# Optimization experiments

Hardware: AMD Instinct MI355X
Metric: run time of the kernel (lower is better)

The kernel has to match this reference:

```python
import jax, jax.numpy as jnp
import numpy as np

V, D, NL, L, N = 50257, 512, 4, 2048, 32  # vocab, d_model, n_layers, seq_len, complex state modes (d_state=64)


def setup_inputs() -> dict:
    key = jax.random.key(0)
    ks = jax.random.split(key, 10)
    s = lambda k, shp, sc=1.0: jax.random.normal(k, shp, dtype=jnp.float32) * sc
    # dt log-uniform in [1e-3, 1e-1], standard S4 init; shared layout (NL, D)
    log_dt = jnp.tile(jnp.linspace(np.log(1e-3), np.log(1e-1), D, dtype=np.float32)[None], (NL, 1))
    return {
        "input_ids": jax.random.randint(ks[0], (2, L), 0, V, dtype=jnp.int64),
        "token_embed": s(ks[1], (V, D), 0.02),
        "pos_embed": s(ks[2], (L, D), 0.02),
        "log_dt": log_dt,
        "C_re": s(ks[3], (NL, D, N)),
        "C_im": s(ks[4], (NL, D, N)),
        "skip_D": s(ks[5], (NL, D)),
        "out_w": s(ks[6], (NL, 2 * D, D), 1.0 / np.sqrt(D)),
        "out_b": jnp.zeros((NL, 2 * D), jnp.float32),
        "ln_g": jnp.ones((D,), jnp.float32),
        "ln_b": jnp.zeros((D,), jnp.float32),
        "head_w": s(ks[7], (V, D), 1.0 / np.sqrt(D)),
    }


def _s4d_kernel(log_dt, C_re, C_im):
    # S4D-Lin init, ZOH discretization -> causal conv kernel (D, L)
    A = (-0.5 + 1j * jnp.pi * jnp.arange(N)).astype(jnp.complex64)      # (N,)
    dtA = jnp.exp(log_dt)[:, None] * A[None, :]                          # (D, N)
    C = (C_re + 1j * C_im).astype(jnp.complex64) * (jnp.exp(dtA) - 1.0) / A
    # Vandermonde: exp(l * dtA); (D, N, L) complex64 transient
    K = C[:, :, None] * jnp.exp(dtA[:, :, None] * jnp.arange(L))
    return 2.0 * jnp.real(K.sum(1))                                      # (D, L)


def _fft_causal_conv(u, K):
    # u: (B, L, D), K: (D, L) -> causal conv along time, per channel
    n = 2 * L
    Uf = jnp.fft.rfft(u, n=n, axis=1)            # (B, n/2+1, D)
    Kf = jnp.fft.rfft(K.T, n=n, axis=0)[None]    # (1, n/2+1, D)
    return jnp.fft.irfft(Uf * Kf, n=n, axis=1)[:, :L]


def _s4_block(x, log_dt, C_re, C_im, skip_D, out_w, out_b):
    y = _fft_causal_conv(x, _s4d_kernel(log_dt, C_re, C_im)) + x * skip_D
    y = jax.nn.gelu(y)
    z = y @ out_w.T + out_b                       # (B, L, 2D)
    return z[..., :D] * jax.nn.sigmoid(z[..., D:])  # GLU output projection


def reference(input_ids, token_embed, pos_embed, log_dt, C_re, C_im,
              skip_D, out_w, out_b, ln_g, ln_b, head_w):
    T = input_ids.shape[1]
    x = token_embed[input_ids] + pos_embed[None, :T]
    for i in range(NL):  # fixed small layer count
        x = x + _s4_block(x, log_dt[i], C_re[i], C_im[i], skip_D[i], out_w[i], out_b[i])
    mu = x.mean(-1, keepdims=True)
    var = ((x - mu) ** 2).mean(-1, keepdims=True)
    x = (x - mu) / jnp.sqrt(var + 1e-5) * ln_g + ln_b
    return x @ head_w.T  # logits (B, L, V)
```

## Files before the change

kernel.cpp:

```cpp
#include <hip/hip_runtime.h>
#include <math.h>

#define LSEQ   2048
#define DM     512
#define NLAYER 4
#define NMODE  32
#define BATCH  2
#define VOCAB  50257
#define CHUNK  32
#define NCHUNK 64
#define ROWS   (BATCH*LSEQ)
#define PI_F   3.14159265358979323846f

typedef __bf16 bf16_t;
typedef __bf16 bf16x8 __attribute__((ext_vector_type(8)));
typedef float  floatx4 __attribute__((ext_vector_type(4)));

__device__ __forceinline__ float gelu_f(float v) {
  return 0.5f * v * (1.0f + tanhf(0.7978845608028654f * (v + 0.044715f * v * v * v)));
}
__device__ __forceinline__ float sigmoid_f(float v) {
  return 1.0f / (1.0f + expf(-v));
}

__global__ __launch_bounds__(256) void prep_kernel(
    const float* __restrict__ log_dt, const float* __restrict__ C_re,
    const float* __restrict__ C_im, float* __restrict__ wcp) {
  int idx = blockIdx.x * 256 + threadIdx.x;
  int n  = idx & (NMODE - 1);
  int ld = idx >> 5;
  float dt = expf(log_dt[ld]);
  float ar = -0.5f * dt;
  float ai = PI_F * (float)n * dt;
  float em = expf(ar);
  float wr = em * cosf(ai), wi = em * sinf(ai);
  float pn = PI_F * (float)n;
  float inv = 1.0f / (0.25f + pn * pn);
  float m1r = wr - 1.0f, m1i = wi;
  float qr = (-0.5f * m1r + pn * m1i) * inv;
  float qi = (-0.5f * m1i - pn * m1r) * inv;
  float cre = C_re[idx], cim = C_im[idx];
  float cpr = cre * qr - cim * qi;
  float cpi = cre * qi + cim * qr;
  float emT = expf(ar * (float)CHUNK);
  float aT  = ai * (float)CHUNK;
  float wTr = emT * cosf(aT), wTi = emT * sinf(aT);
  float* o = wcp + (size_t)idx * 6;
  o[0] = wr; o[1] = wi; o[2] = cpr; o[3] = cpi; o[4] = wTr; o[5] = wTi;
}

__global__ __launch_bounds__(256) void embed_kernel(
    const int* __restrict__ ids, const float* __restrict__ tok,
    const float* __restrict__ pos, float* __restrict__ x) {
  int idx = blockIdx.x * 256 + threadIdx.x;
  int d  = idx & (DM - 1);
  int bl = idx >> 9;
  int l  = bl & (LSEQ - 1);
  int id = ids[bl];
  x[idx] = tok[(size_t)id * DM + d] + pos[(size_t)l * DM + d];
}

__global__ __launch_bounds__(256) void cvt_bf16_kernel(
    const float* __restrict__ src, bf16_t* __restrict__ dst, int n) {
  int idx = blockIdx.x * 256 + threadIdx.x;
  if (idx < n) dst[idx] = (bf16_t)src[idx];
}

__global__ __launch_bounds__(256) void scan_phase1_kernel(
    const float* __restrict__ x, const float* __restrict__ wcp,
    float2* __restrict__ E, int layer) {
  int idx = blockIdx.x * 256 + threadIdx.x;
  int d  = idx & (DM - 1);
  int bc = idx >> 9;
  int c  = bc & (NCHUNK - 1);
  int b  = bc >> 6;
  const float* xp = x + ((size_t)(b * LSEQ + c * CHUNK)) * DM + d;
  float xr[CHUNK];
  #pragma unroll
  for (int t = 0; t < CHUNK; t++) xr[t] = xp[(size_t)t * DM];
  const float* wp = wcp + (size_t)(layer * DM + d) * NMODE * 6;
  float2* Ep = E + ((size_t)(b * DM + d) * NCHUNK + c) * NMODE;
  #pragma unroll 1
  for (int np = 0; np < NMODE / 2; np++) {
    int n0 = np * 2;
    float w0r = wp[n0*6+0], w0i = wp[n0*6+1];
    float w1r = wp[n0*6+6], w1i = wp[n0*6+7];
    float s0r = 0.f, s0i = 0.f, s1r = 0.f, s1i = 0.f;
    #pragma unroll
    for (int t = 0; t < CHUNK; t++) {
      float xt = xr[t];
      float a0r = fmaf(w0r, s0r, fmaf(-w0i, s0i, xt));
      float a0i = fmaf(w0r, s0i, w0i * s0r);
      float a1r = fmaf(w1r, s1r, fmaf(-w1i, s1i, xt));
      float a1i = fmaf(w1r, s1i, w1i * s1r);
      s0r = a0r; s0i = a0i; s1r = a1r; s1i = a1i;
    }
    Ep[n0]     = make_float2(s0r, s0i);
    Ep[n0 + 1] = make_float2(s1r, s1i);
  }
}

__global__ __launch_bounds__(256) void scan_combine_kernel(
    const float* __restrict__ wcp, float2* __restrict__ E, int layer) {
  int idx = blockIdx.x * 256 + threadIdx.x;
  int n  = idx & (NMODE - 1);
  int bd = idx >> 5;
  int d  = bd & (DM - 1);
  const float* wp = wcp + ((size_t)(layer * DM + d) * NMODE + n) * 6;
  float wTr = wp[4], wTi = wp[5];
  float2* Ep = E + (size_t)bd * NCHUNK * NMODE + n;
  float sr = 0.f, si = 0.f;
  for (int c = 0; c < NCHUNK; c++) {
    float2 e = Ep[(size_t)c * NMODE];
    Ep[(size_t)c * NMODE] = make_float2(sr, si);
    float tr = fmaf(wTr, sr, -(wTi * si)) + e.x;
    float ti = fmaf(wTr, si, wTi * sr) + e.y;
    sr = tr; si = ti;
  }
}

__global__ __launch_bounds__(256) void scan_phase2_kernel(
    const float* __restrict__ x, const float* __restrict__ wcp,
    const float2* __restrict__ E, const float* __restrict__ skipD,
    bf16_t* __restrict__ yb, int layer) {
  int idx = blockIdx.x * 256 + threadIdx.x;
  int d  = idx & (DM - 1);
  int bc = idx >> 9;
  int c  = bc & (NCHUNK - 1);
  int b  = bc >> 6;
  const float* xp = x + ((size_t)(b * LSEQ + c * CHUNK)) * DM + d;
  float xr[CHUNK];
  #pragma unroll
  for (int t = 0; t < CHUNK; t++) xr[t] = xp[(size_t)t * DM];
  float ya[CHUNK];
  #pragma unroll
  for (int t = 0; t < CHUNK; t++) ya[t] = 0.f;
  const float* wp = wcp + (size_t)(layer * DM + d) * NMODE * 6;
  const float2* Ep = E + ((size_t)(b * DM + d) * NCHUNK + c) * NMODE;
  #pragma unroll 1
  for (int np = 0; np < NMODE / 2; np++) {
    int n0 = np * 2;
    float w0r = wp[n0*6+0], w0i = wp[n0*6+1];
    float c0r = wp[n0*6+2], c0i = wp[n0*6+3];
    float w1r = wp[n0*6+6], w1i = wp[n0*6+7];
    float c1r = wp[n0*6+8], c1i = wp[n0*6+9];
    float2 e0 = Ep[n0], e1 = Ep[n0 + 1];
    float s0r = e0.x, s0i = e0.y, s1r = e1.x, s1i = e1.y;
    #pragma unroll
    for (int t = 0; t < CHUNK; t++) {
      float xt = xr[t];
      float a0r = fmaf(w0r, s0r, fmaf(-w0i, s0i, xt));
      float a0i = fmaf(w0r, s0i, w0i * s0r);
      float a1r = fmaf(w1r, s1r, fmaf(-w1i, s1i, xt));
      float a1i = fmaf(w1r, s1i, w1i * s1r);
      s0r = a0r; s0i = a0i; s1r = a1r; s1i = a1i;
      float acc = fmaf(c0r, s0r, ya[t]);
      acc = fmaf(-c0i, s0i, acc);
      acc = fmaf(c1r, s1r, acc);
      ya[t] = fmaf(-c1i, s1i, acc);
    }
  }
  float sk = skipD[layer * DM + d];
  bf16_t* yp = yb + ((size_t)(b * LSEQ + c * CHUNK)) * DM + d;
  #pragma unroll
  for (int t = 0; t < CHUNK; t++) {
    float v = fmaf(xr[t], sk, 2.0f * ya[t]);
    yp[(size_t)t * DM] = (bf16_t)gelu_f(v);
  }
}

__global__ __launch_bounds__(256) void gemm_bt_kernel(
    const bf16_t* __restrict__ A, const bf16_t* __restrict__ B,
    float* __restrict__ C, const float* __restrict__ bias, int Nreal, int K) {
  __shared__ __align__(16) bf16_t As[128 * 32];
  __shared__ __align__(16) bf16_t Bs[128 * 32];
  int tid = threadIdx.x;
  int lid = tid & 63;
  int w   = tid >> 6;
  int tileM = blockIdx.y * 128;
  int tileN = blockIdx.x * 128;
  int wm = w & 1, wn = w >> 1;

  floatx4 acc[4][4];
  floatx4 zero = {0.f, 0.f, 0.f, 0.f};
  #pragma unroll
  for (int i = 0; i < 4; i++)
    #pragma unroll
    for (int j = 0; j < 4; j++) acc[i][j] = zero;

  for (int k0 = 0; k0 < K; k0 += 32) {
    #pragma unroll
    for (int i = 0; i < 2; i++) {
      int flat = i * 256 + tid;
      int row  = flat >> 2;
      int kg   = (flat & 3) * 8;
      const bf16_t* ga = A + (size_t)(tileM + row) * K + (k0 + kg);
      int brow = tileN + row;
      if (brow >= Nreal) brow = Nreal - 1;
      const bf16_t* gb = B + (size_t)brow * K + (k0 + kg);
      __builtin_amdgcn_global_load_lds(
          (const __attribute__((address_space(1))) void*)ga,
          (__attribute__((address_space(3))) void*)(&As[flat * 8]), 16, 0, 0);
      __builtin_amdgcn_global_load_lds(
          (const __attribute__((address_space(1))) void*)gb,
          (__attribute__((address_space(3))) void*)(&Bs[flat * 8]), 16, 0, 0);
    }
    __syncthreads();

    bf16x8 af[4], bfr[4];
    #pragma unroll
    for (int i = 0; i < 4; i++) {
      af[i]  = *(const bf16x8*)&As[((wm * 64 + i * 16 + (lid & 15)) * 32) + ((lid >> 4) * 8)];
      bfr[i] = *(const bf16x8*)&Bs[((wn * 64 + i * 16 + (lid & 15)) * 32) + ((lid >> 4) * 8)];
    }
    #pragma unroll
    for (int i = 0; i < 4; i++)
      #pragma unroll
      for (int j = 0; j < 4; j++)
        acc[i][j] = __builtin_amdgcn_mfma_f32_16x16x32_bf16(af[i], bfr[j], acc[i][j], 0, 0, 0);
    __syncthreads();
  }

  #pragma unroll
  for (int i = 0; i < 4; i++) {
    int m = tileM + wm * 64 + i * 16 + (lid >> 4) * 4;
    #pragma unroll
    for (int j = 0; j < 4; j++) {
      int n = tileN + wn * 64 + j * 16 + (lid & 15);
      if (n < Nreal) {
        float bv = bias ? bias[n] : 0.f;
        #pragma unroll
        for (int r = 0; r < 4; r++)
          C[(size_t)(m + r) * Nreal + n] = acc[i][j][r] + bv;
      }
    }
  }
}

__global__ __launch_bounds__(256) void glu_res_kernel(
    const float* __restrict__ z, float* __restrict__ x) {
  int idx = blockIdx.x * 256 + threadIdx.x;
  int d = idx & (DM - 1);
  int m = idx >> 9;
  float a = z[(size_t)m * (2 * DM) + d];
  float g = z[(size_t)m * (2 * DM) + DM + d];
  x[idx] += a * sigmoid_f(g);
}

__global__ __launch_bounds__(256) void ln_kernel(
    const float* __restrict__ x, const float* __restrict__ g,
    const float* __restrict__ bta, bf16_t* __restrict__ xn) {
  int m = blockIdx.x;
  int tid = threadIdx.x;
  int lid = tid & 63, w = tid >> 6;
  const float* xp = x + (size_t)m * DM;
  float v0 = xp[tid], v1 = xp[tid + 256];
  __shared__ float sw[4];
  __shared__ float bcast;
  float s = v0 + v1;
  #pragma unroll
  for (int o = 32; o > 0; o >>= 1) s += __shfl_down(s, o);
  if (lid == 0) sw[w] = s;
  __syncthreads();
  if (tid == 0) bcast = (sw[0] + sw[1] + sw[2] + sw[3]) * (1.0f / DM);
  __syncthreads();
  float mu = bcast;
  float d0 = v0 - mu, d1 = v1 - mu;
  float q = d0 * d0 + d1 * d1;
  #pragma unroll
  for (int o = 32; o > 0; o >>= 1) q += __shfl_down(q, o);
  __syncthreads();
  if (lid == 0) sw[w] = q;
  __syncthreads();
  if (tid == 0) bcast = rsqrtf((sw[0] + sw[1] + sw[2] + sw[3]) * (1.0f / DM) + 1e-5f);
  __syncthreads();
  float rs = bcast;
  xn[(size_t)m * DM + tid]       = (bf16_t)(d0 * rs * g[tid] + bta[tid]);
  xn[(size_t)m * DM + tid + 256] = (bf16_t)(d1 * rs * g[tid + 256] + bta[tid + 256]);
}

extern "C" void kernel_launch(void* const* d_in, const int* in_sizes, int n_in,
                              void* d_out, int out_size, void* d_ws, size_t ws_size,
                              hipStream_t stream) {
  const int*   ids   = (const int*)  d_in[0];
  const float* tok   = (const float*)d_in[1];
  const float* pos   = (const float*)d_in[2];
  const float* logdt = (const float*)d_in[3];
  const float* cre   = (const float*)d_in[4];
  const float* cim   = (const float*)d_in[5];
  const float* skipD = (const float*)d_in[6];
  const float* outw  = (const float*)d_in[7];
  const float* outb  = (const float*)d_in[8];
  const float* lng   = (const float*)d_in[9];
  const float* lnb   = (const float*)d_in[10];
  const float* headw = (const float*)d_in[11];
  float* logits = (float*)d_out;

  char* ws = (char*)d_ws;
  float*  x   = (float*)(ws);
  float*  z   = (float*)(ws + (8u  << 20));
  float2* E   = (float2*)(ws + (8u << 20));
  bf16_t* yb  = (bf16_t*)(ws + (24u << 20));
  bf16_t* xn  = (bf16_t*)(ws + (24u << 20));
  bf16_t* wb  = (bf16_t*)(ws + (28u << 20));
  float*  wcp = (float*)(ws + (32u << 20));
  bf16_t* hb  = (bf16_t*)(ws + (34u << 20));

  prep_kernel<<<(NLAYER * DM * NMODE) / 256, 256, 0, stream>>>(logdt, cre, cim, wcp);
  cvt_bf16_kernel<<<(NLAYER * 2 * DM * DM) / 256, 256, 0, stream>>>(outw, wb, NLAYER * 2 * DM * DM);
  cvt_bf16_kernel<<<(VOCAB * DM + 255) / 256, 256, 0, stream>>>(headw, hb, VOCAB * DM);
  embed_kernel<<<(ROWS * DM) / 256, 256, 0, stream>>>(ids, tok, pos, x);

  for (int layer = 0; layer < NLAYER; layer++) {
    scan_phase1_kernel<<<(BATCH * NCHUNK * DM) / 256, 256, 0, stream>>>(x, wcp, E, layer);
    scan_combine_kernel<<<(BATCH * DM * NMODE) / 256, 256, 0, stream>>>(wcp, E, layer);
    scan_phase2_kernel<<<(BATCH * NCHUNK * DM) / 256, 256, 0, stream>>>(x, wcp, E, skipD, yb, layer);
    dim3 g1((2 * DM) / 128, ROWS / 128);
    gemm_bt_kernel<<<g1, 256, 0, stream>>>(yb, wb + (size_t)layer * 2 * DM * DM, z,
                                           outb + layer * 2 * DM, 2 * DM, DM);
    glu_res_kernel<<<(ROWS * DM) / 256, 256, 0, stream>>>(z, x);
  }

  ln_kernel<<<ROWS, 256, 0, stream>>>(x, lng, lnb, xn);
  dim3 g2((VOCAB + 127) / 128, ROWS / 128);
  gemm_bt_kernel<<<g2, 256, 0, stream>>>(xn, hb, logits, nullptr, VOCAB, DM);
}
```

Before: 1.583 ms.

## Fuse GLU into output-projection GEMM, retile head GEMM, vectorize bf16 conversions

Each layer's output-projection GEMM now applies the GLU gate and residual add in its epilogue. The weight rows are permuted at conversion time so gate and value columns land in the same tile, which removes the z buffer round trip and one kernel per layer. The vocab head GEMM moves to a 256x256 tile, 512-thread kernel with 64-wide K double-buffered LDS staging, an XCD-aware block remap and MFMA priority hints. The fp32-to-bf16 conversions are vectorized to 8 elements per thread. The risks are the larger LDS footprint (128KB per block) limiting occupancy, and correctness of the row permutation.

```diff
diff --git a/kernel.cpp b/kernel.cpp
--- a/kernel.cpp
+++ b/kernel.cpp
@@ -60,10 +60,35 @@
   x[idx] = tok[(size_t)id * DM + d] + pos[(size_t)l * DM + d];
 }
 
-__global__ __launch_bounds__(256) void cvt_bf16_kernel(
-    const float* __restrict__ src, bf16_t* __restrict__ dst, int n) {
-  int idx = blockIdx.x * 256 + threadIdx.x;
-  if (idx < n) dst[idx] = (bf16_t)src[idx];
+__global__ __launch_bounds__(256) void cvt8_kernel(
+    const float* __restrict__ src, bf16_t* __restrict__ dst, int n8) {
+  int idx8 = blockIdx.x * 256 + threadIdx.x;
+  if (idx8 >= n8) return;
+  int gid = idx8 * 8;
+  float4 f0 = *(const float4*)(src + gid);
+  float4 f1 = *(const float4*)(src + gid + 4);
+  bf16x8 v;
+  v[0] = (bf16_t)f0.x; v[1] = (bf16_t)f0.y; v[2] = (bf16_t)f0.z; v[3] = (bf16_t)f0.w;
+  v[4] = (bf16_t)f1.x; v[5] = (bf16_t)f1.y; v[6] = (bf16_t)f1.z; v[7] = (bf16_t)f1.w;
+  *(bf16x8*)(dst + gid) = v;
+}
+
+__global__ __launch_bounds__(256) void cvt_wperm_kernel(
+    const float* __restrict__ src, bf16_t* __restrict__ dst) {
+  int idx8 = blockIdx.x * 256 + threadIdx.x;
+  int gid = idx8 * 8;
+  int layer = gid >> 19;
+  int rem = gid & ((1 << 19) - 1);
+  int r = rem >> 9;
+  int c = rem & 511;
+  int orig = ((r >> 4) & 1) * 512 + ((r >> 5) << 4) + (r & 15);
+  const float* s = src + ((size_t)layer << 19) + ((size_t)orig << 9) + c;
+  float4 f0 = *(const float4*)s;
+  float4 f1 = *(const float4*)(s + 4);
+  bf16x8 v;
+  v[0] = (bf16_t)f0.x; v[1] = (bf16_t)f0.y; v[2] = (bf16_t)f0.z; v[3] = (bf16_t)f0.w;
+  v[4] = (bf16_t)f1.x; v[5] = (bf16_t)f1.y; v[6] = (bf16_t)f1.z; v[7] = (bf16_t)f1.w;
+  *(bf16x8*)(dst + gid) = v;
 }
 
 __global__ __launch_bounds__(256) void scan_phase1_kernel(
@@ -169,9 +194,9 @@
   }
 }
 
-__global__ __launch_bounds__(256) void gemm_bt_kernel(
+__global__ __launch_bounds__(256) void gemm1_glu_kernel(
     const bf16_t* __restrict__ A, const bf16_t* __restrict__ B,
-    float* __restrict__ C, const float* __restrict__ bias, int Nreal, int K) {
+    const float* __restrict__ bias2, float* __restrict__ x) {
   __shared__ __align__(16) bf16_t As[128 * 32];
   __shared__ __align__(16) bf16_t Bs[128 * 32];
   int tid = threadIdx.x;
@@ -188,63 +213,151 @@
     #pragma unroll
     for (int j = 0; j < 4; j++) acc[i][j] = zero;
 
-  for (int k0 = 0; k0 < K; k0 += 32) {
+  for (int k0 = 0; k0 < DM; k0 += 32) {
     #pragma unroll
     for (int i = 0; i < 2; i++) {
       int flat = i * 256 + tid;
       int row  = flat >> 2;
       int kg   = (flat & 3) * 8;
+      const bf16_t* ga = A + (size_t)(tileM + row) * DM + (k0 + kg);
+      const bf16_t* gb = B + (size_t)(tileN + row) * DM + (k0 + kg);
+      __builtin_amdgcn_global_load_lds(
+          (const __attribute__((address_space(1))) void*)ga,
+          (__attribute__((address_space(3))) void*)(&As[flat * 8]), 16, 0, 0);
+      __builtin_amdgcn_global_load_lds(
+          (const __attribute__((address_space(1))) void*)gb,
+          (__attribute__((address_space(3))) void*)(&Bs[flat * 8]), 16, 0, 0);
+    }
+    __syncthreads();
+
+    bf16x8 af[4], bfr[4];
+    #pragma unroll
+    for (int i = 0; i < 4; i++) {
+      af[i]  = *(const bf16x8*)&As[((wm * 64 + i * 16 + (lid & 15)) * 32) + ((lid >> 4) * 8)];
+      bfr[i] = *(const bf16x8*)&Bs[((wn * 64 + i * 16 + (lid & 15)) * 32) + ((lid >> 4) * 8)];
+    }
+    #pragma unroll
+    for (int i = 0; i < 4; i++)
+      #pragma unroll
+      for (int j = 0; j < 4; j++)
+        acc[i][j] = __builtin_amdgcn_mfma_f32_16x16x32_bf16(af[i], bfr[j], acc[i][j], 0, 0, 0);
+    __syncthreads();
+  }
+
+  #pragma unroll
+  for (int i = 0; i < 4; i++) {
+    int m = tileM + wm * 64 + i * 16 + (lid >> 4) * 4;
+    #pragma unroll
+    for (int j = 0; j < 4; j += 2) {
+      int n0 = tileN + wn * 64 + j * 16;
+      int d  = ((n0 >> 5) << 4) + (lid & 15);
+      float ba = bias2[d], bg = bias2[512 + d];
+      #pragma unroll
+      for (int r = 0; r < 4; r++) {
+        float a = acc[i][j][r] + ba;
+        float g = acc[i][j + 1][r] + bg;
+        size_t xi = (size_t)(m + r) * DM + d;
+        x[xi] += a * sigmoid_f(g);
+      }
+    }
+  }
+}
+
+__global__ __launch_bounds__(512, 2) void gemm_head_kernel(
+    const bf16_t* __restrict__ A, const bf16_t* __restrict__ B,
+    float* __restrict__ C, int Nreal) {
+  __shared__ __align__(16) bf16_t As0[256 * 64];
+  __shared__ __align__(16) bf16_t Bs0[256 * 64];
+  __shared__ __align__(16) bf16_t As1[256 * 64];
+  __shared__ __align__(16) bf16_t Bs1[256 * 64];
+  const int K = DM;
+  int tid = threadIdx.x;
+  int lid = tid & 63;
+  int w   = tid >> 6;
+  int wm  = w >> 2, wn = w & 3;
+
+  int nwg = gridDim.x;
+  int bid = blockIdx.x;
+  int xcd = bid & 7, lin = bid >> 3;
+  int q = nwg >> 3, rq = nwg & 7;
+  int wgid = (xcd < rq ? xcd * (q + 1) : rq * (q + 1) + (xcd - rq) * q) + lin;
+  int tileM = (wgid & 15) * 256;
+  int tileN = (wgid >> 4) * 256;
+
+  floatx4 acc[8][4];
+  floatx4 zero = {0.f, 0.f, 0.f, 0.f};
+  #pragma unroll
+  for (int i = 0; i < 8; i++)
+    #pragma unroll
+    for (int j = 0; j < 4; j++) acc[i][j] = zero;
+
+  auto STAGE = [&](bf16_t* as, bf16_t* bs, int k0) {
+    #pragma unroll
+    for (int i = 0; i < 4; i++) {
+      int flat = i * 512 + tid;
+      int row  = flat >> 3;
+      int kg   = (flat & 7) * 8;
       const bf16_t* ga = A + (size_t)(tileM + row) * K + (k0 + kg);
       int brow = tileN + row;
       if (brow >= Nreal) brow = Nreal - 1;
       const bf16_t* gb = B + (size_t)brow * K + (k0 + kg);
       __builtin_amdgcn_global_load_lds(
           (const __attribute__((address_space(1))) void*)ga,
-          (__attribute__((address_space(3))) void*)(&As[flat * 8]), 16, 0, 0);
+          (__attribute__((address_space(3))) void*)(&as[flat * 8]), 16, 0, 0);
       __builtin_amdgcn_global_load_lds(
           (const __attribute__((address_space(1))) void*)gb,
-          (__attribute__((address_space(3))) void*)(&Bs[flat * 8]), 16, 0, 0);
-    }
-    __syncthreads();
-
-    bf16x8 af[4], bfr[4];
-    #pragma unroll
-    for (int i = 0; i < 4; i++) {
-      af[i]  = *(const bf16x8*)&As[((wm * 64 + i * 16 + (lid & 15)) * 32) + ((lid >> 4) * 8)];
-      bfr[i] = *(const bf16x8*)&Bs[((wn * 64 + i * 16 + (lid & 15)) * 32) + ((lid >> 4) * 8)];
-    }
-    #pragma unroll
-    for (int i = 0; i < 4; i++)
+          (__attribute__((address_space(3))) void*)(&bs[flat * 8]), 16, 0, 0);
+    }
+  };
+
+  auto COMPUTE = [&](const bf16_t* as, const bf16_t* bs) {
+    #pragma unroll
+    for (int ks = 0; ks < 2; ks++) {
+      bf16x8 af[8], bfr[4];
+      #pragma unroll
+      for (int i = 0; i < 8; i++)
+        af[i] = *(const bf16x8*)&as[(wm * 128 + i * 16 + (lid & 15)) * 64 + ks * 32 + (lid >> 4) * 8];
       #pragma unroll
       for (int j = 0; j < 4; j++)
-        acc[i][j] = __builtin_amdgcn_mfma_f32_16x16x32_bf16(af[i], bfr[j], acc[i][j], 0, 0, 0);
+        bfr[j] = *(const bf16x8*)&bs[(wn * 64 + j * 16 + (lid & 15)) * 64 + ks * 32 + (lid >> 4) * 8];
+      __builtin_amdgcn_s_setprio(1);
+      #pragma unroll
+      for (int i = 0; i < 8; i++)
+        #pragma unroll
+        for (int j = 0; j < 4; j++)
+          acc[i][j] = __builtin_amdgcn_mfma_f32_16x16x32_bf16(af[i], bfr[j], acc[i][j], 0, 0, 0);
+      __builtin_amdgcn_s_setprio(0);
+    }
+  };
+
+  const int nt = K >> 6;
+  STAGE(As0, Bs0, 0);
+  __syncthreads();
+  #pragma unroll 1
+  for (int t = 0; t < nt; t += 2) {
+    if (t + 1 < nt) STAGE(As1, Bs1, (t + 1) << 6);
+    COMPUTE(As0, Bs0);
     __syncthreads();
-  }
-
-  #pragma unroll
-  for (int i = 0; i < 4; i++) {
-    int m = tileM + wm * 64 + i * 16 + (lid >> 4) * 4;
+    if (t + 1 < nt) {
+      if (t + 2 < nt) STAGE(As0, Bs0, (t + 2) << 6);
+      COMPUTE(As1, Bs1);
+      __syncthreads();
+    }
+  }
+
+  #pragma unroll
+  for (int i = 0; i < 8; i++) {
+    int m = tileM + wm * 128 + i * 16 + (lid >> 4) * 4;
     #pragma unroll
     for (int j = 0; j < 4; j++) {
       int n = tileN + wn * 64 + j * 16 + (lid & 15);
       if (n < Nreal) {
-        float bv = bias ? bias[n] : 0.f;
         #pragma unroll
         for (int r = 0; r < 4; r++)
-          C[(size_t)(m + r) * Nreal + n] = acc[i][j][r] + bv;
+          C[(size_t)(m + r) * Nreal + n] = acc[i][j][r];
       }
     }
   }
-}
-
-__global__ __launch_bounds__(256) void glu_res_kernel(
-    const float* __restrict__ z, float* __restrict__ x) {
-  int idx = blockIdx.x * 256 + threadIdx.x;
-  int d = idx & (DM - 1);
-  int m = idx >> 9;
-  float a = z[(size_t)m * (2 * DM) + d];
-  float g = z[(size_t)m * (2 * DM) + DM + d];
-  x[idx] += a * sigmoid_f(g);
 }
 
 __global__ __launch_bounds__(256) void ln_kernel(
@@ -266,11 +379,11 @@
   __syncthreads();
   float mu = bcast;
   float d0 = v0 - mu, d1 = v1 - mu;
-  float q = d0 * d0 + d1 * d1;
-  #pragma unroll
-  for (int o = 32; o > 0; o >>= 1) q += __shfl_down(q, o);
-  __syncthreads();
-  if (lid == 0) sw[w] = q;
+  float qq = d0 * d0 + d1 * d1;
+  #pragma unroll
+  for (int o = 32; o > 0; o >>= 1) qq += __shfl_down(qq, o);
+  __syncthreads();
+  if (lid == 0) sw[w] = qq;
   __syncthreads();
   if (tid == 0) bcast = rsqrtf((sw[0] + sw[1] + sw[2] + sw[3]) * (1.0f / DM) + 1e-5f);
   __syncthreads();
@@ -298,17 +411,17 @@
 
   char* ws = (char*)d_ws;
   float*  x   = (float*)(ws);
-  float*  z   = (float*)(ws + (8u  << 20));
-  float2* E   = (float2*)(ws + (8u << 20));
+  float2* E   = (float2*)(ws + (8u  << 20));
   bf16_t* yb  = (bf16_t*)(ws + (24u << 20));
   bf16_t* xn  = (bf16_t*)(ws + (24u << 20));
-  bf16_t* wb  = (bf16_t*)(ws + (28u << 20));
+  bf16_t* wbp = (bf16_t*)(ws + (28u << 20));
   float*  wcp = (float*)(ws + (32u << 20));
   bf16_t* hb  = (bf16_t*)(ws + (34u << 20));
 
   prep_kernel<<<(NLAYER * DM * NMODE) / 256, 256, 0, stream>>>(logdt, cre, cim, wcp);
-  cvt_bf16_kernel<<<(NLAYER * 2 * DM * DM) / 256, 256, 0, stream>>>(outw, wb, NLAYER * 2 * DM * DM);
-  cvt_bf16_kernel<<<(VOCAB * DM + 255) / 256, 256, 0, stream>>>(headw, hb, VOCAB * DM);
+  cvt_wperm_kernel<<<(NLAYER * 2 * DM * DM / 8) / 256, 256, 0, stream>>>(outw, wbp);
+  int n8 = (VOCAB * DM) / 8;
+  cvt8_kernel<<<(n8 + 255) / 256, 256, 0, stream>>>(headw, hb, n8);
   embed_kernel<<<(ROWS * DM) / 256, 256, 0, stream>>>(ids, tok, pos, x);
 
   for (int layer = 0; layer < NLAYER; layer++) {
@@ -316,12 +429,11 @@
     scan_combine_kernel<<<(BATCH * DM * NMODE) / 256, 256, 0, stream>>>(wcp, E, layer);
     scan_phase2_kernel<<<(BATCH * NCHUNK * DM) / 256, 256, 0, stream>>>(x, wcp, E, skipD, yb, layer);
     dim3 g1((2 * DM) / 128, ROWS / 128);
-    gemm_bt_kernel<<<g1, 256, 0, stream>>>(yb, wb + (size_t)layer * 2 * DM * DM, z,
-                                           outb + layer * 2 * DM, 2 * DM, DM);
-    glu_res_kernel<<<(ROWS * DM) / 256, 256, 0, stream>>>(z, x);
+    gemm1_glu_kernel<<<g1, 256, 0, stream>>>(yb, wbp + (size_t)layer * 2 * DM * DM,
+                                             outb + layer * 2 * DM, x);
   }
 
   ln_kernel<<<ROWS, 256, 0, stream>>>(x, lng, lnb, xn);
-  dim3 g2((VOCAB + 127) / 128, ROWS / 128);
-  gemm_bt_kernel<<<g2, 256, 0, stream>>>(xn, hb, logits, nullptr, VOCAB, DM);
-}
+  int ntn = (VOCAB + 255) / 256;
+  gemm_head_kernel<<<16 * ntn, 512, 0, stream>>>(xn, hb, logits, VOCAB);
+}
```

After: 1.739 ms. 9.8% more time.
